# Performance work log

Hardware: AMD Instinct MI355X
Metric: run time of the kernel (lower is better)

The kernel has to match this reference:

```python
import jax, jax.numpy as jnp
import numpy as np

N_STRIDE = 128  # 'n' from __init__: stride between subsequences


def make_mask(S, m, n):
    # Faithful vectorization of create_mask: overlap of windows [i*n, i*n+m).
    # overlap_ratio = max(0, m - |i-j|*n) / m; mask True iff (0.5 <= ratio < 1) or i == j.
    # (ratio >= 1 only happens at i == j, which the first branch already catches.)
    idx = jnp.arange(S)
    diff = jnp.abs(idx[:, None] - idx[None, :])
    ratio = jnp.maximum(0, m - diff * n).astype(jnp.float32) / m
    return ((ratio >= 0.5) & (ratio < 1.0)) | (diff == 0)


def setup_inputs() -> dict:
    key = jax.random.key(0)
    k1, k2, k3 = jax.random.split(key, 3)
    B, D, S, L = 8, 8, 512, 256  # batch, num_dims, num_subsequences, seq_length(=d_model)
    x = jax.random.normal(k1, (B, D, S, L), jnp.float32)
    qkv_w = jax.random.normal(k2, (3 * L, L), jnp.float32) * (1.0 / np.sqrt(L))
    qkv_b = jax.random.normal(k3, (3 * L,), jnp.float32) * 0.02
    return {"x": x, "qkv_w": qkv_w, "qkv_b": qkv_b}


def reference(x, qkv_w, qkv_b):
    B, D, S, L = x.shape
    # Batched over the per-channel Python loop in the original.
    qkv = jnp.einsum('bdsl,ol->bdso', x, qkv_w) + qkv_b  # [B,D,S,3L]
    q, k, v = jnp.split(qkv, 3, axis=-1)
    attn = jnp.einsum('bdsh,bdth->bdst', q, k) / jnp.sqrt(jnp.float32(L))
    attn = jax.nn.softmax(attn, axis=-1)
    mask = make_mask(S, L, N_STRIDE)  # m = d_model = L
    attn = jnp.where(mask, jnp.float32(0), attn)  # masked_fill(mask, 0)
    out = jnp.einsum('bdst,bdth->bdsh', attn, v).reshape(B, D * S, L)
    # Block-diagonal scatter of per-channel attention maps: [B, D*S, D*S]
    z = jnp.zeros((B, D, S, D, S), attn.dtype)
    z = z.at[:, jnp.arange(D), :, jnp.arange(D), :].set(jnp.transpose(attn, (1, 0, 2, 3)))
    block = z.reshape(B, D * S, D * S)
    return out, block
```

## Files before the change

### kernel.cpp

```cpp
#include <hip/hip_runtime.h>

typedef unsigned short u16;
typedef __attribute__((ext_vector_type(8))) short bf16x8;
typedef __attribute__((ext_vector_type(4))) float f32x4;

#define NS 512
#define NL 256
#define NBD 64
#define OUT_ELEMS 8388608u

__device__ __forceinline__ u16 f2bf(float f) {
  union { float f; unsigned u; } v; v.f = f;
  unsigned u = v.u;
  unsigned r = (u + 0x7FFFu + ((u >> 16) & 1u)) >> 16;
  return (u16)r;
}

__device__ __forceinline__ bf16x8 pack8(float4 a, float4 b) {
  bf16x8 r;
  r[0] = (short)f2bf(a.x); r[1] = (short)f2bf(a.y);
  r[2] = (short)f2bf(a.z); r[3] = (short)f2bf(a.w);
  r[4] = (short)f2bf(b.x); r[5] = (short)f2bf(b.y);
  r[6] = (short)f2bf(b.z); r[7] = (short)f2bf(b.w);
  return r;
}

__global__ __launch_bounds__(256) void qkv_kernel(
    const float* __restrict__ x, const float* __restrict__ w,
    const float* __restrict__ bias,
    u16* __restrict__ qws, u16* __restrict__ kws, u16* __restrict__ vws)
{
  __shared__ u16 wlds[64][264];

  const int t = threadIdx.x;
  const int wave = t >> 6, lane = t & 63;
  const int r16 = lane & 15, kg = lane >> 4;
  const int row0 = blockIdx.x * 64;
  const int srow = row0 + wave * 16 + r16;

  bf16x8 a[8];
  {
    const float* xr = x + (size_t)srow * NL;
    for (int ks = 0; ks < 8; ++ks) {
      float4 f0 = *(const float4*)(xr + ks * 32 + kg * 8);
      float4 f1 = *(const float4*)(xr + ks * 32 + kg * 8 + 4);
      a[ks] = pack8(f0, f1);
    }
  }

  const int wr = t >> 2, qq = t & 3;
  for (int ct = 0; ct < 12; ++ct) {
    const int col0 = ct * 64;
    __syncthreads();
    {
      const float* src = w + (size_t)(col0 + wr) * NL + qq * 64;
      u16* dst = &wlds[wr][qq * 64];
      for (int j = 0; j < 64; j += 8) {
        float4 f0 = *(const float4*)(src + j);
        float4 f1 = *(const float4*)(src + j + 4);
        *(bf16x8*)(void*)(dst + j) = pack8(f0, f1);
      }
    }
    __syncthreads();

    for (int cf = 0; cf < 4; ++cf) {
      const int cl = cf * 16 + r16;
      f32x4 acc = {0.f, 0.f, 0.f, 0.f};
      for (int ks = 0; ks < 8; ++ks) {
        bf16x8 b = *(const bf16x8*)(void*)&wlds[cl][ks * 32 + kg * 8];
        acc = __builtin_amdgcn_mfma_f32_16x16x32_bf16(a[ks], b, acc, 0, 0, 0);
      }
      const int o = col0 + cl;
      const float bv = bias[o];
      for (int i = 0; i < 4; ++i) {
        const float val = acc[i] + bv;
        const int grow = row0 + wave * 16 + kg * 4 + i;
        const int bd = grow >> 9, s = grow & 511;
        const u16 h = f2bf(val);
        if (o < 256)      qws[((size_t)bd * NS + s) * NL + o] = h;
        else if (o < 512) kws[((size_t)bd * NS + s) * NL + (o - 256)] = h;
        else              vws[((size_t)bd * NL + (o - 512)) * NS + s] = h;
      }
    }
  }
}

__global__ __launch_bounds__(256) void attn_kernel(
    const u16* __restrict__ qws, const u16* __restrict__ kws,
    const u16* __restrict__ vws, float* __restrict__ out)
{
  __shared__ float Sm[32][516];
  __shared__ float red[32][8];
  __shared__ float rowstat[32];

  const int rt = blockIdx.x, bd = blockIdx.y;
  const int b = bd >> 3, d = bd & 7;
  const int t = threadIdx.x, wave = t >> 6, lane = t & 63;
  const int r16 = lane & 15, kg = lane >> 4;
  const size_t ch = (size_t)bd * NS * NL;

  bf16x8 aq[2][8];
  for (int rf = 0; rf < 2; ++rf) {
    const int s1 = rt * 32 + rf * 16 + r16;
    const u16* p = qws + ch + (size_t)s1 * NL + kg * 8;
    for (int ks = 0; ks < 8; ++ks)
      aq[rf][ks] = *(const bf16x8*)(p + ks * 32);
  }

  for (int cf = 0; cf < 8; ++cf) {
    const int s2 = wave * 128 + cf * 16 + r16;
    const u16* p = kws + ch + (size_t)s2 * NL + kg * 8;
    f32x4 acc0 = {0, 0, 0, 0}, acc1 = {0, 0, 0, 0};
    for (int ks = 0; ks < 8; ++ks) {
      bf16x8 bfr = *(const bf16x8*)(p + ks * 32);
      acc0 = __builtin_amdgcn_mfma_f32_16x16x32_bf16(aq[0][ks], bfr, acc0, 0, 0, 0);
      acc1 = __builtin_amdgcn_mfma_f32_16x16x32_bf16(aq[1][ks], bfr, acc1, 0, 0, 0);
    }
    const int c = wave * 128 + cf * 16 + r16;
    for (int i = 0; i < 4; ++i) {
      Sm[kg * 4 + i][c]      = acc0[i] * 0.0625f;
      Sm[16 + kg * 4 + i][c] = acc1[i] * 0.0625f;
    }
  }
  __syncthreads();

  const int r = t >> 3, c8 = t & 7;
  float m = -1e30f;
  for (int j = 0; j < 8; ++j)
    for (int u = 0; u < 8; ++u)
      m = fmaxf(m, Sm[r][c8 * 8 + j * 64 + u]);
  red[r][c8] = m;
  __syncthreads();
  if (t < 32) {
    float mm = red[t][0];
    for (int j = 1; j < 8; ++j) mm = fmaxf(mm, red[t][j]);
    rowstat[t] = mm;
  }
  __syncthreads();
  const float rm = rowstat[r];
  float ssum = 0.f;
  for (int j = 0; j < 8; ++j)
    for (int u = 0; u < 8; ++u) {
      const int c = c8 * 8 + j * 64 + u;
      const float e = __expf(Sm[r][c] - rm);
      Sm[r][c] = e;
      ssum += e;
    }
  red[r][c8] = ssum;
  __syncthreads();
  if (t < 32) {
    float s = 0.f;
    for (int j = 0; j < 8; ++j) s += red[t][j];
    rowstat[t] = 1.0f / s;
  }
  __syncthreads();

  const float inv = rowstat[r];
  const int s1g = rt * 32 + r;
  float* brow = out + OUT_ELEMS + ((size_t)b << 24) +
                (size_t)(d * NS + s1g) * 4096 + d * NS;
  for (int j = 0; j < 8; ++j) {
    const int cbase = c8 * 8 + j * 64;
    float vals[8];
    for (int u = 0; u < 8; ++u) {
      const int c = cbase + u;
      float v = Sm[r][c] * inv;
      const int dd = c > s1g ? c - s1g : s1g - c;
      if (dd <= 1) v = 0.f;
      Sm[r][c] = v;
      vals[u] = v;
    }
    *(float4*)(brow + cbase)     = *(float4*)vals;
    *(float4*)(brow + cbase + 4) = *(float4*)(vals + 4);
  }
  __syncthreads();

  f32x4 accO[2][4];
  for (int rf = 0; rf < 2; ++rf)
    for (int cf = 0; cf < 4; ++cf) accO[rf][cf] = (f32x4){0, 0, 0, 0};
  for (int ks = 0; ks < 16; ++ks) {
    bf16x8 pa[2];
    for (int rf = 0; rf < 2; ++rf) {
      const float* p = &Sm[rf * 16 + r16][ks * 32 + kg * 8];
      pa[rf] = pack8(*(const float4*)p, *(const float4*)(p + 4));
    }
    for (int cf = 0; cf < 4; ++cf) {
      const int f = wave * 64 + cf * 16 + r16;
      bf16x8 bv = *(const bf16x8*)(vws + ((size_t)bd * NL + f) * NS + ks * 32 + kg * 8);
      accO[0][cf] = __builtin_amdgcn_mfma_f32_16x16x32_bf16(pa[0], bv, accO[0][cf], 0, 0, 0);
      accO[1][cf] = __builtin_amdgcn_mfma_f32_16x16x32_bf16(pa[1], bv, accO[1][cf], 0, 0, 0);
    }
  }
  for (int rf = 0; rf < 2; ++rf)
    for (int cf = 0; cf < 4; ++cf) {
      const int fcol = wave * 64 + cf * 16 + r16;
      for (int i = 0; i < 4; ++i) {
        const int s1 = rt * 32 + rf * 16 + kg * 4 + i;
        out[(size_t)b * (4096u * 256u) + (size_t)(d * NS + s1) * NL + fcol] =
            accO[rf][cf][i];
      }
    }
}

extern "C" void kernel_launch(void* const* d_in, const int* in_sizes, int n_in,
                              void* d_out, int out_size, void* d_ws, size_t ws_size,
                              hipStream_t stream) {
  const float* x    = (const float*)d_in[0];
  const float* w    = (const float*)d_in[1];
  const float* bias = (const float*)d_in[2];
  float* out = (float*)d_out;

  u16* qws = (u16*)d_ws;
  u16* kws = qws + (size_t)NBD * NS * NL;
  u16* vws = kws + (size_t)NBD * NS * NL;

  hipMemsetAsync(d_out, 0, (size_t)out_size * sizeof(float), stream);

  qkv_kernel<<<dim3(512), 256, 0, stream>>>(x, w, bias, qws, kws, vws);
  attn_kernel<<<dim3(16, 64), 256, 0, stream>>>(qws, kws, vws, out);
}
```

Before: 296.6 us.

## Fuse zero-fill of block-diagonal output into attention kernel with nontemporal stores

Removes the full-output hipMemsetAsync and instead has each attention block zero the off-diagonal parts of its own 32 rows of the block matrix, skipping the diagonal block it writes itself. The attention-map writes and zero writes use nontemporal stores to avoid polluting cache. This avoids writing the diagonal region twice and saves a separate memset pass, but adds store traffic inside the attention kernel that may compete with its compute.

```diff
diff --git a/kernel.cpp b/kernel.cpp
--- a/kernel.cpp
+++ b/kernel.cpp
@@ -22,6 +22,15 @@
   r[2] = (short)f2bf(a.z); r[3] = (short)f2bf(a.w);
   r[4] = (short)f2bf(b.x); r[5] = (short)f2bf(b.y);
   r[6] = (short)f2bf(b.z); r[7] = (short)f2bf(b.w);
+  return r;
+}
+
+__device__ __forceinline__ bf16x8 pack8v(f32x4 a, f32x4 b) {
+  bf16x8 r;
+  r[0] = (short)f2bf(a[0]); r[1] = (short)f2bf(a[1]);
+  r[2] = (short)f2bf(a[2]); r[3] = (short)f2bf(a[3]);
+  r[4] = (short)f2bf(b[0]); r[5] = (short)f2bf(b[1]);
+  r[6] = (short)f2bf(b[2]); r[7] = (short)f2bf(b[3]);
   return r;
 }
 
@@ -99,6 +108,18 @@
   const int r16 = lane & 15, kg = lane >> 4;
   const size_t ch = (size_t)bd * NS * NL;
 
+  {
+    const f32x4 z4 = {0.f, 0.f, 0.f, 0.f};
+    float* base = out + OUT_ELEMS + ((size_t)b << 24) +
+                  (size_t)(d * NS + rt * 32) * 4096;
+    const int dlo = d << 7;
+    for (int idx = t; idx < 32 * 1024; idx += 256) {
+      const int row = idx >> 10, c4 = idx & 1023;
+      if ((unsigned)(c4 - dlo) >= 128u)
+        __builtin_nontemporal_store(z4, (f32x4*)(base + (size_t)row * 4096) + c4);
+    }
+  }
+
   bf16x8 aq[2][8];
   for (int rf = 0; rf < 2; ++rf) {
     const int s1 = rt * 32 + rf * 16 + r16;
@@ -161,17 +182,25 @@
                 (size_t)(d * NS + s1g) * 4096 + d * NS;
   for (int j = 0; j < 8; ++j) {
     const int cbase = c8 * 8 + j * 64;
-    float vals[8];
-    for (int u = 0; u < 8; ++u) {
+    f32x4 v0, v1;
+    for (int u = 0; u < 4; ++u) {
       const int c = cbase + u;
       float v = Sm[r][c] * inv;
       const int dd = c > s1g ? c - s1g : s1g - c;
       if (dd <= 1) v = 0.f;
       Sm[r][c] = v;
-      vals[u] = v;
-    }
-    *(float4*)(brow + cbase)     = *(float4*)vals;
-    *(float4*)(brow + cbase + 4) = *(float4*)(vals + 4);
+      v0[u] = v;
+    }
+    for (int u = 0; u < 4; ++u) {
+      const int c = cbase + 4 + u;
+      float v = Sm[r][c] * inv;
+      const int dd = c > s1g ? c - s1g : s1g - c;
+      if (dd <= 1) v = 0.f;
+      Sm[r][c] = v;
+      v1[u] = v;
+    }
+    __builtin_nontemporal_store(v0, (f32x4*)(brow + cbase));
+    __builtin_nontemporal_store(v1, (f32x4*)(brow + cbase + 4));
   }
   __syncthreads();
 
@@ -182,7 +211,7 @@
     bf16x8 pa[2];
     for (int rf = 0; rf < 2; ++rf) {
       const float* p = &Sm[rf * 16 + r16][ks * 32 + kg * 8];
-      pa[rf] = pack8(*(const float4*)p, *(const float4*)(p + 4));
+      pa[rf] = pack8v(*(const f32x4*)p, *(const f32x4*)(p + 4));
     }
     for (int cf = 0; cf < 4; ++cf) {
       const int f = wave * 64 + cf * 16 + r16;
@@ -214,8 +243,6 @@
   u16* kws = qws + (size_t)NBD * NS * NL;
   u16* vws = kws + (size_t)NBD * NS * NL;
 
-  hipMemsetAsync(d_out, 0, (size_t)out_size * sizeof(float), stream);
-
   qkv_kernel<<<dim3(512), 256, 0, stream>>>(x, w, bias, qws, kws, vws);
   attn_kernel<<<dim3(16, 64), 256, 0, stream>>>(qws, kws, vws, out);
 }
```

New measurement: 274.0 us. 1.08x faster.
